# Optimization experiments

Measured on AMD Instinct MI355X. Metric: run time of the kernel, lower is better.

## Reference

```python
import jax, jax.numpy as jnp
import numpy as np

DIM = 384
HEADS = 12
WS = (2, 7, 7)
SS = (1, 3, 3)


def _rel_position_index(ws):
    coords = np.stack(np.meshgrid(np.arange(ws[0]), np.arange(ws[1]), np.arange(ws[2]), indexing='ij'))
    cf = coords.reshape(3, -1)                      # (3, N)
    rc = cf[:, :, None] - cf[:, None, :]            # (3, N, N)
    rc = rc.transpose(1, 2, 0).astype(np.int64)     # (N, N, 3)
    rc[..., 0] += ws[0] - 1
    rc[..., 1] += ws[1] - 1
    rc[..., 2] += ws[2] - 1
    rc[..., 0] *= (2 * ws[1] - 1) * (2 * ws[2] - 1)
    rc[..., 1] *= 2 * ws[2] - 1
    return rc.sum(-1)                               # (N, N)


def _compute_mask(D, H, W, ws, ss):
    img = np.zeros((1, D, H, W, 1), np.float32)
    cnt = 0
    for d in (slice(0, -ws[0]), slice(-ws[0], -ss[0]), slice(-ss[0], None)):
        for h in (slice(0, -ws[1]), slice(-ws[1], -ss[1]), slice(-ss[1], None)):
            for w in (slice(0, -ws[2]), slice(-ws[2], -ss[2]), slice(-ss[2], None)):
                img[:, d, h, w, :] = cnt
                cnt += 1
    x = img.reshape(1, D // ws[0], ws[0], H // ws[1], ws[1], W // ws[2], ws[2], 1)
    mw = x.transpose(0, 1, 3, 5, 2, 4, 6, 7).reshape(-1, ws[0] * ws[1] * ws[2])  # (nW, N)
    am = mw[:, None, :] - mw[:, :, None]
    return jnp.asarray(np.where(am != 0, -100.0, 0.0).astype(np.float32))  # (nW, N, N)


def _window_partition(x, ws):
    B, D, H, W, C = x.shape
    x = x.reshape(B, D // ws[0], ws[0], H // ws[1], ws[1], W // ws[2], ws[2], C)
    return x.transpose(0, 1, 3, 5, 2, 4, 6, 7).reshape(-1, ws[0] * ws[1] * ws[2], C)


def _window_reverse(win, ws, B, D, H, W):
    x = win.reshape(B, D // ws[0], H // ws[1], W // ws[2], ws[0], ws[1], ws[2], -1)
    return x.transpose(0, 1, 4, 2, 5, 3, 6, 7).reshape(B, D, H, W, -1)


def _ln(x, g, b, eps=1e-5):
    mu = x.mean(-1, keepdims=True)
    var = ((x - mu) ** 2).mean(-1, keepdims=True)
    return (x - mu) * jax.lax.rsqrt(var + eps) * g + b


def setup_inputs() -> dict:
    key = jax.random.key(0)
    ks = jax.random.split(key, 8)
    C = DIM
    Ch = int(4.0 * C)
    s = lambda k, shape: jax.random.normal(k, shape, dtype=jnp.float32) * 0.02
    nbias = (2 * WS[0] - 1) * (2 * WS[1] - 1) * (2 * WS[2] - 1)
    return dict(
        x=jax.random.normal(ks[0], (4, 8, 56, 56, C), dtype=jnp.float32),
        norm1_g=jnp.ones((C,), jnp.float32), norm1_b=jnp.zeros((C,), jnp.float32),
        qkv_w=s(ks[1], (3 * C, C)), qkv_b=jnp.zeros((3 * C,), jnp.float32),
        rpb_table=s(ks[2], (nbias, HEADS)),
        proj_w=s(ks[3], (C, C)), proj_b=jnp.zeros((C,), jnp.float32),
        norm2_g=jnp.ones((C,), jnp.float32), norm2_b=jnp.zeros((C,), jnp.float32),
        fc1_w=s(ks[4], (Ch, C)), fc1_b=jnp.zeros((Ch,), jnp.float32),
        fc2_w=s(ks[5], (C, Ch)), fc2_b=jnp.zeros((C,), jnp.float32),
    )


def reference(x, norm1_g, norm1_b, qkv_w, qkv_b, rpb_table, proj_w, proj_b,
              norm2_g, norm2_b, fc1_w, fc1_b, fc2_w, fc2_b):
    B, D, H, W, C = x.shape
    ws, ss = WS, SS
    hd = C // HEADS
    N = ws[0] * ws[1] * ws[2]

    shortcut = x
    h = _ln(x, norm1_g, norm1_b)
    # cyclic shift (no padding needed: D,H,W are window multiples)
    h = jnp.roll(h, shift=(-ss[0], -ss[1], -ss[2]), axis=(1, 2, 3))
    xw = _window_partition(h, ws)                       # (B_, N, C)
    B_ = xw.shape[0]

    qkv = (xw @ qkv_w.T + qkv_b).reshape(B_, N, 3, HEADS, hd).transpose(2, 0, 3, 1, 4)
    q, k, v = qkv[0], qkv[1], qkv[2]                    # (B_, heads, N, hd)
    attn = jnp.einsum('bhnd,bhmd->bhnm', q * (hd ** -0.5), k)

    rpi = _rel_position_index(ws)                       # (N, N) static
    bias = rpb_table[rpi.reshape(-1)].reshape(N, N, HEADS).transpose(2, 0, 1)
    attn = attn + bias[None]

    mask = _compute_mask(D, H, W, ws, ss)               # (nW, N, N)
    nW = mask.shape[0]
    attn = attn.reshape(B_ // nW, nW, HEADS, N, N) + mask[None, :, None]
    attn = jax.nn.softmax(attn.reshape(-1, HEADS, N, N), axis=-1)

    out = jnp.einsum('bhnm,bhmd->bhnd', attn, v).transpose(0, 2, 1, 3).reshape(B_, N, C)
    out = out @ proj_w.T + proj_b

    h = _window_reverse(out, ws, B, D, H, W)
    h = jnp.roll(h, shift=(ss[0], ss[1], ss[2]), axis=(1, 2, 3))
    x = shortcut + h

    y = _ln(x, norm2_g, norm2_b)
    y = jax.nn.gelu(y @ fc1_w.T + fc1_b, approximate=False) @ fc2_w.T + fc2_b
    return x + y
```

## Files before the change

kernel.cpp:

```cpp
#include <hip/hip_runtime.h>
#include <hip/hip_bf16.h>
#include <cmath>

typedef __hip_bfloat16 bf16;
typedef __attribute__((ext_vector_type(8))) short s16x8;
typedef __attribute__((ext_vector_type(4))) float f32x4v;

__device__ __forceinline__ float bf2f(bf16 v){ return __bfloat162float(v); }
__device__ __forceinline__ bf16  f2bf(float v){ return __float2bfloat16(v); }

__device__ __forceinline__ void gload16(const void* g, void* l){
  __builtin_amdgcn_global_load_lds((const __attribute__((address_space(1))) void*)g,
                                   (__attribute__((address_space(3))) void*)l,
                                   16, 0, 0);
}

__device__ __forceinline__ int xcd_swizzle(int bid, int nb){
  int q = nb >> 3, r = nb & 7;
  int xcd = bid & 7, idx = bid >> 3;
  return (xcd < r) ? (xcd*(q+1) + idx) : (r + xcd*q + idx);
}

__device__ __forceinline__ float gelu_f(float v){
  float y = 0.797884561f*(v + 0.044715f*v*v*v);
  float e = __expf(-2.f*y);
  return v * __builtin_amdgcn_rcpf(1.f + e);
}

__global__ void k_f2bf4(const float* __restrict__ s0, const float* __restrict__ s1,
                        const float* __restrict__ s2, const float* __restrict__ s3,
                        bf16* __restrict__ out){
  int i = blockIdx.x*256 + threadIdx.x;
  if (i >= 1769472) return;
  float v;
  if      (i <  442368) v = s0[i];
  else if (i <  589824) v = s1[i -  442368];
  else if (i < 1179648) v = s2[i -  589824];
  else                  v = s3[i - 1179648];
  out[i] = f2bf(v);
}

__global__ void k_comb(const float* __restrict__ rpb, float* __restrict__ comb){
  int idx = blockIdx.x*256 + threadIdx.x;
  int col = idx & 127, row = (idx>>7)&127, clshead = idx>>14;
  int cls = clshead/12, head = clshead - cls*12;
  float v;
  if (row >= 98) v = 0.f;
  else if (col >= 98) v = -10000.f;
  else {
    int qd = row/49, qr = row%49, qh = qr/7, qw = qr%7;
    int kd = col/49, kr = col%49, kh = kr/7, kw = kr%7;
    int pbq = qd*169 + qh*13 + qw;
    int pbk = kd*169 + kh*13 + kw;
    int lq, lk;
    {
      int ld = (cls&4) ? (qd==0?1:2) : 0;
      int lh = (cls&2) ? (qh<4?1:2) : 0;
      int lw = (cls&1) ? (qw<4?1:2) : 0;
      lq = ld*9+lh*3+lw;
    }
    {
      int ld = (cls&4) ? (kd==0?1:2) : 0;
      int lh = (cls&2) ? (kh<4?1:2) : 0;
      int lw = (cls&1) ? (kw<4?1:2) : 0;
      lk = ld*9+lh*3+lw;
    }
    float bias = rpb[(pbq-pbk+253)*12 + head];
    v = bias + ((lq!=lk) ? -100.f : 0.f);
  }
  comb[idx] = v;
}

__global__ __launch_bounds__(256)
void k_ln1(const float* __restrict__ x, const float* __restrict__ g,
           const float* __restrict__ b, bf16* __restrict__ xw, long tbase)
{
  int tl = blockIdx.x*4 + (threadIdx.x>>6);
  long t = tbase + tl;
  int lane = threadIdx.x & 63;
  int win = (int)(t / 98), n = (int)(t % 98);
  int batch = win>>8;
  int wq = win & 7, hq = (win>>3)&7, dq = (win>>6)&3;
  int dr = n/49, rem = n%49, hr = rem/7, wr = rem%7;
  int d = dq*2+dr, h = hq*7+hr, w = wq*7+wr;
  int sd = (d+1)&7;
  int sh = h+3; if (sh>=56) sh-=56;
  int sw = w+3; if (sw>=56) sw-=56;
  const float* row = x + ((size_t)(((batch*8+sd)*56+sh)*56+sw))*384;
  float v[6]; float s=0.f, ss=0.f;
  int c0 = lane*6;
  #pragma unroll
  for (int i=0;i<6;++i){ float f = row[c0+i]; v[i]=f; s+=f; ss+=f*f; }
  #pragma unroll
  for (int o=32;o>0;o>>=1){ s += __shfl_xor(s,o); ss += __shfl_xor(ss,o); }
  float mu = s*(1.f/384.f);
  float var = ss*(1.f/384.f) - mu*mu;
  float rstd = rsqrtf(var + 1e-5f);
  bf16* orow = xw + (size_t)tl*384;
  #pragma unroll
  for (int i=0;i<6;++i){ int c=c0+i; orow[c] = f2bf((v[i]-mu)*rstd*g[c] + b[c]); }
}

template<int EPI, int KT>
__global__ __launch_bounds__(256, 2)
void k_gemm(const bf16* __restrict__ A, const bf16* __restrict__ B,
            const float* __restrict__ bias, const float* __restrict__ resid,
            void* __restrict__ outp, int N, int nx)
{
  constexpr int K = KT*32;
  __shared__ __align__(16) bf16 As[2][256*32];
  __shared__ __align__(16) bf16 Bs[2][128*32];
  const int tid = threadIdx.x;
  const int wave = tid>>6, lane = tid&63;
  const int wg = xcd_swizzle(blockIdx.x, gridDim.x);
  const int tn = wg % nx, tm = wg / nx;
  const int wm = wave>>1, wn = wave&1;
  const int fr = lane & 15, l4 = lane>>4;

  f32x4v acc[8][4];
  #pragma unroll
  for (int i=0;i<8;++i)
    #pragma unroll
    for (int j=0;j<4;++j)
      #pragma unroll
      for (int e=0;e<4;++e) acc[i][j][e] = 0.f;

  const int srow0 = lane>>2;
  const int scol_sw = (((lane&3) ^ ((lane>>3)&3)))*8;
  const bf16* gA = A + ((size_t)tm*256 + wave*16 + srow0)*K + scol_sw;
  const bf16* gB = B + ((size_t)tn*128 + wave*16 + srow0)*K + scol_sw;

  auto stage = [&](int buf, int koff){
    #pragma unroll
    for (int j=0;j<4;++j)
      gload16(gA + (size_t)(64*j)*K + koff, &As[buf][j*2048 + wave*512]);
    #pragma unroll
    for (int j=0;j<2;++j)
      gload16(gB + (size_t)(64*j)*K + koff, &Bs[buf][j*2048 + wave*512]);
  };

  stage(0, 0);

  const int fko_sw = ((l4 ^ ((fr>>1)&3)))*8;

  #pragma unroll 2
  for (int kt=0; kt<KT; ++kt){
    asm volatile("s_waitcnt vmcnt(0) lgkmcnt(0)" ::: "memory");
    __builtin_amdgcn_s_barrier();
    if (kt+1 < KT) stage((kt+1)&1, (kt+1)*32);
    const bf16* Ab = As[kt&1];
    const bf16* Bb = Bs[kt&1];
    s16x8 af[8], bfr[4];
    #pragma unroll
    for (int i=0;i<4;++i)
      bfr[i] = *(const s16x8*)&Bb[(wn*64 + i*16 + fr)*32 + fko_sw];
    #pragma unroll
    for (int i=0;i<8;++i)
      af[i] = *(const s16x8*)&Ab[(wm*128 + i*16 + fr)*32 + fko_sw];
    #pragma unroll
    for (int mi=0;mi<8;++mi)
      #pragma unroll
      for (int ni=0;ni<4;++ni)
        acc[mi][ni] = __builtin_amdgcn_mfma_f32_16x16x32_bf16(af[mi], bfr[ni], acc[mi][ni], 0,0,0);
    __builtin_amdgcn_s_barrier();
  }

  #pragma unroll
  for (int mi=0;mi<8;++mi){
    #pragma unroll
    for (int ni=0;ni<4;++ni){
      int col = tn*128 + wn*64 + ni*16 + fr;
      float bv = bias[col];
      int rowb = tm*256 + wm*128 + mi*16 + l4*4;
      #pragma unroll
      for (int r=0;r<4;++r){
        size_t idx = (size_t)(rowb+r)*N + col;
        float v = acc[mi][ni][r] + bv;
        if (EPI==0){
          ((bf16*)outp)[idx] = f2bf(v);
        } else if (EPI==1){
          ((bf16*)outp)[idx] = f2bf(gelu_f(v));
        } else if (EPI==3){
          if (col < 384) v *= 0.17677669529663687f;
          ((bf16*)outp)[idx] = f2bf(v);
        } else {
          ((float*)outp)[idx] = v + resid[idx];
        }
      }
    }
  }
}

template<int KT>
__global__ __launch_bounds__(512, 1)
void k_projln2(const bf16* __restrict__ A, const bf16* __restrict__ B,
               const float* __restrict__ bias, const float* __restrict__ x,
               const float* __restrict__ g, const float* __restrict__ b2,
               float* __restrict__ outx, bf16* __restrict__ ln2,
               long tbase, long lnbase)
{
  constexpr int K = KT*32;
  __shared__ __align__(16) bf16 As[2][128*32];
  __shared__ __align__(16) bf16 Bs[2][384*32];
  __shared__ float redS[128][4];
  __shared__ float redQ[128][4];
  const int tid = threadIdx.x;
  const int wave = tid>>6, lane = tid&63;
  const int tm = xcd_swizzle(blockIdx.x, gridDim.x);
  const int wm = wave>>2, wn = wave&3;
  const int fr = lane & 15, l4 = lane>>4;

  f32x4v acc[4][6];
  #pragma unroll
  for (int i=0;i<4;++i)
    #pragma unroll
    for (int j=0;j<6;++j)
      #pragma unroll
      for (int e=0;e<4;++e) acc[i][j][e] = 0.f;

  const int srow0 = lane>>2;
  const int scol_sw = (((lane&3) ^ ((lane>>3)&3)))*8;
  const bf16* gA = A + ((size_t)tm*128 + wave*16 + srow0)*K + scol_sw;
  const bf16* gB = B + ((size_t)(wave*16) + srow0)*K + scol_sw;

  auto stage = [&](int buf, int koff){
    gload16(gA + koff, &As[buf][wave*512]);
    #pragma unroll
    for (int j=0;j<3;++j)
      gload16(gB + (size_t)(128*j)*K + koff, &Bs[buf][(j*128 + wave*16)*32]);
  };

  stage(0, 0);
  const int fko_sw = ((l4 ^ ((fr>>1)&3)))*8;

  #pragma unroll 2
  for (int kt=0; kt<KT; ++kt){
    asm volatile("s_waitcnt vmcnt(0) lgkmcnt(0)" ::: "memory");
    __builtin_amdgcn_s_barrier();
    if (kt+1 < KT) stage((kt+1)&1, (kt+1)*32);
    const bf16* Ab = As[kt&1];
    const bf16* Bb = Bs[kt&1];
    s16x8 af[4], bfr[6];
    #pragma unroll
    for (int i=0;i<6;++i)
      bfr[i] = *(const s16x8*)&Bb[(wn*96 + i*16 + fr)*32 + fko_sw];
    #pragma unroll
    for (int i=0;i<4;++i)
      af[i] = *(const s16x8*)&Ab[(wm*64 + i*16 + fr)*32 + fko_sw];
    #pragma unroll
    for (int mi=0;mi<4;++mi)
      #pragma unroll
      for (int ni=0;ni<6;++ni)
        acc[mi][ni] = __builtin_amdgcn_mfma_f32_16x16x32_bf16(af[mi], bfr[ni], acc[mi][ni], 0,0,0);
    __builtin_amdgcn_s_barrier();
  }

  float bv[6];
  #pragma unroll
  for (int ni=0;ni<6;++ni) bv[ni] = bias[wn*96 + ni*16 + fr];

  long nr[4][4];
  #pragma unroll
  for (int mi=0;mi<4;++mi){
    #pragma unroll
    for (int r=0;r<4;++r){
      int lrow = wm*64 + mi*16 + l4*4 + r;
      int ti = (int)(tbase + (long)tm*128 + lrow);
      int win = ti/98, n = ti - win*98;
      int batch = win>>8;
      int wq = win&7, hq = (win>>3)&7, dq = (win>>6)&3;
      int dr = n/49, rem = n - dr*49, hr = rem/7, wr = rem - hr*7;
      int d = dq*2+dr, h = hq*7+hr, w = wq*7+wr;
      int sd = (d+1)&7;
      int sh = h+3; if (sh>=56) sh-=56;
      int sw = w+3; if (sw>=56) sw-=56;
      long nrow = (long)batch*25088 + (long)(sd*56+sh)*56 + sw;
      nr[mi][r] = nrow;
      const float* xrow = x + (size_t)nrow*384;
      float* orow = outx + (size_t)nrow*384;
      float s = 0.f, q = 0.f;
      #pragma unroll
      for (int ni=0;ni<6;++ni){
        int col = wn*96 + ni*16 + fr;
        float hvl = acc[mi][ni][r] + bv[ni] + xrow[col];
        orow[col] = hvl;
        acc[mi][ni][r] = hvl;
        s += hvl; q += hvl*hvl;
      }
      s += __shfl_xor(s,1); q += __shfl_xor(q,1);
      s += __shfl_xor(s,2); q += __shfl_xor(q,2);
      s += __shfl_xor(s,4); q += __shfl_xor(q,4);
      s += __shfl_xor(s,8); q += __shfl_xor(q,8);
      if (fr == 0){ redS[lrow][wn] = s; redQ[lrow][wn] = q; }
    }
  }
  __syncthreads();
  float gv[6], b2v[6];
  #pragma unroll
  for (int ni=0;ni<6;++ni){
    int col = wn*96 + ni*16 + fr;
    gv[ni] = g[col]; b2v[ni] = b2[col];
  }
  #pragma unroll
  for (int mi=0;mi<4;++mi){
    #pragma unroll
    for (int r=0;r<4;++r){
      int lrow = wm*64 + mi*16 + l4*4 + r;
      float S = redS[lrow][0] + redS[lrow][1] + redS[lrow][2] + redS[lrow][3];
      float Q = redQ[lrow][0] + redQ[lrow][1] + redQ[lrow][2] + redQ[lrow][3];
      float mu = S*(1.f/384.f);
      float var = Q*(1.f/384.f) - mu*mu;
      float rstd = rsqrtf(var + 1e-5f);
      bf16* lrowp = ln2 + (size_t)(nr[mi][r] - lnbase)*384;
      #pragma unroll
      for (int ni=0;ni<6;++ni){
        int col = wn*96 + ni*16 + fr;
        lrowp[col] = f2bf((acc[mi][ni][r] - mu)*rstd*gv[ni] + b2v[ni]);
      }
    }
  }
}

__global__ __launch_bounds__(256)
void k_attn(const bf16* __restrict__ qkv, const float* __restrict__ comb,
            bf16* __restrict__ outp)
{
  const int wg   = xcd_swizzle(blockIdx.x, gridDim.x);
  const int head = wg % 12;
  const int win  = wg / 12;
  const int tid  = threadIdx.x;
  const int wave = tid>>6;
  const int lane = tid&63;
  const int l15 = lane & 15, l4 = lane>>4;
  __shared__ __align__(16) bf16 Vt[32*136];
  __shared__ __align__(16) bf16 P_buf[4][16*40];

  const int wq = win&7, hq=(win>>3)&7, dq=(win>>6)&3;
  const int cls = ((dq==3)?4:0) | ((hq==7)?2:0) | ((wq==7)?1:0);
  const float* combbase = comb + (size_t)(cls*12+head)*128*128;
  const bf16* qkvw_ = qkv + (size_t)win*98*1152;

  for (int i = tid; i < 512; i += 256){
    int m = i>>2, d0 = (i&3)*8;
    int mc = m>97 ? 97 : m;
    s16x8 v = *(const s16x8*)(qkvw_ + (size_t)mc*1152 + 384 + 384 + head*32 + d0);
    #pragma unroll
    for (int e=0;e<8;++e){ short sv = v[e]; Vt[(d0+e)*136 + m] = *(bf16*)&sv; }
  }
  s16x8 kb[8];
  #pragma unroll
  for (int j=0;j<8;++j){
    int tok = j*16 + l15; if (tok>97) tok = 97;
    kb[j] = *(const s16x8*)(qkvw_ + (size_t)tok*1152 + 384 + head*32 + l4*8);
  }
  __syncthreads();

  const int c0 = wave*32;
  bf16* Pw = P_buf[wave];
  #pragma unroll
  for (int mi=0;mi<2;++mi){
    int q = c0 + mi*16 + l15; if (q>97) q=97;
    s16x8 aq = *(const s16x8*)(qkvw_ + (size_t)q*1152 + head*32 + l4*8);
    f32x4v s[8];
    const float* cb = combbase + (size_t)(c0+mi*16+l4*4)*128 + l15;
    #pragma unroll
    for (int j=0;j<8;++j){
      f32x4v ci = { cb[j*16], cb[j*16+128], cb[j*16+256], cb[j*16+384] };
      s[j] = __builtin_amdgcn_mfma_f32_16x16x32_bf16(aq, kb[j], ci, 0,0,0);
    }
    float rinv[4];
    #pragma unroll
    for (int r=0;r<4;++r){
      float mx = s[0][r];
      #pragma unroll
      for (int j=1;j<8;++j) mx = fmaxf(mx, s[j][r]);
      mx = fmaxf(mx, __shfl_xor(mx,1));
      mx = fmaxf(mx, __shfl_xor(mx,2));
      mx = fmaxf(mx, __shfl_xor(mx,4));
      mx = fmaxf(mx, __shfl_xor(mx,8));
      float sum = 0.f;
      #pragma unroll
      for (int j=0;j<8;++j){ float e = __expf(s[j][r]-mx); s[j][r]=e; sum+=e; }
      sum += __shfl_xor(sum,1);
      sum += __shfl_xor(sum,2);
      sum += __shfl_xor(sum,4);
      sum += __shfl_xor(sum,8);
      rinv[r] = 1.f/sum;
    }
    f32x4v oacc[2] = {{0.f,0.f,0.f,0.f},{0.f,0.f,0.f,0.f}};
    #pragma unroll
    for (int ks=0; ks<4; ++ks){
      #pragma unroll
      for (int jj=0;jj<2;++jj)
        #pragma unroll
        for (int r=0;r<4;++r)
          Pw[(l4*4+r)*40 + jj*16 + l15] = f2bf(s[ks*2+jj][r]);
      s16x8 pa = *(const s16x8*)&Pw[l15*40 + l4*8];
      #pragma unroll
      for (int ni=0;ni<2;++ni){
        s16x8 vb = *(const s16x8*)&Vt[(ni*16+l15)*136 + ks*32 + l4*8];
        oacc[ni] = __builtin_amdgcn_mfma_f32_16x16x32_bf16(pa, vb, oacc[ni], 0,0,0);
      }
    }
    #pragma unroll
    for (int r=0;r<4;++r){
      int qo = c0 + mi*16 + l4*4 + r;
      if (qo < 98){
        bf16* orow = outp + ((size_t)win*98 + qo)*384 + head*32;
        #pragma unroll
        for (int ni=0;ni<2;++ni)
          orow[ni*16+l15] = f2bf(oacc[ni][r]*rinv[r]);
      }
    }
  }
}

extern "C" void kernel_launch(void* const* d_in, const int* in_sizes, int n_in,
                              void* d_out, int out_size, void* d_ws, size_t ws_size,
                              hipStream_t stream)
{
  const float* x     = (const float*)d_in[0];
  const float* n1g   = (const float*)d_in[1];
  const float* n1b   = (const float*)d_in[2];
  const float* qkvw  = (const float*)d_in[3];
  const float* qkvbv = (const float*)d_in[4];
  const float* rpb   = (const float*)d_in[5];
  const float* projw = (const float*)d_in[6];
  const float* projb = (const float*)d_in[7];
  const float* n2g   = (const float*)d_in[8];
  const float* n2b   = (const float*)d_in[9];
  const float* fc1w  = (const float*)d_in[10];
  const float* fc1b  = (const float*)d_in[11];
  const float* fc2w  = (const float*)d_in[12];
  const float* fc2b  = (const float*)d_in[13];
  float* out = (float*)d_out;

  char* ws = (char*)d_ws;
  size_t off = 0;
  auto alloc = [&](size_t bytes)->char*{
    char* p = ws + off; off += (bytes + 255) & ~(size_t)255; return p;
  };
  bf16*  wall  = (bf16*)alloc((size_t)1769472*2);
  bf16*  wqkv  = wall;
  bf16*  wproj = wall + 442368;
  bf16*  wfc1  = wall + 589824;
  bf16*  wfc2  = wall + 1179648;
  float* comb  = (float*)alloc((size_t)96*128*128*4);

  k_f2bf4<<<(1769472+255)/256,256,0,stream>>>(qkvw, projw, fc1w, fc2w, wall);
  k_comb<<<6144,256,0,stream>>>(rpb, comb);

  const size_t fused_need = off
      + (((size_t)100352*384*2  + 255) & ~(size_t)255)
      + (((size_t)100352*1536*2 + 255) & ~(size_t)255)
      + (((size_t)100352*384*2  + 255) & ~(size_t)255);
  if (ws_size >= fused_need){
    bf16* xw   = (bf16*)alloc((size_t)100352*384*2);
    bf16* bufA = (bf16*)alloc((size_t)100352*1536*2);
    bf16* ln2  = (bf16*)alloc((size_t)100352*384*2);
    bf16* attno = bufA + (size_t)100352*1152;

    k_ln1<<<25088,256,0,stream>>>(x, n1g, n1b, xw, 0L);
    k_gemm<3,12><<<392*9,256,0,stream>>>(xw, wqkv, qkvbv, nullptr, bufA, 1152, 9);
    k_attn<<<12*1024,256,0,stream>>>(bufA, comb, attno);
    k_projln2<12><<<784,512,0,stream>>>(attno, wproj, projb, x, n2g, n2b, out, ln2, 0L, 0L);
    k_gemm<1,12><<<392*12,256,0,stream>>>(ln2, wfc1, fc1b, nullptr, bufA, 1536, 12);
    k_gemm<2,48><<<392*3,256,0,stream>>>(bufA, wfc2, fc2b, out, (void*)out, 384, 3);
  } else {
    bf16* xw   = (bf16*)alloc((size_t)25088*384*2);
    bf16* bufA = (bf16*)alloc((size_t)25088*1536*2);
    bf16* ln2  = (bf16*)alloc((size_t)25088*384*2);
    bf16* attno = bufA + (size_t)25088*1152;
    for (int b=0; b<4; ++b){
      long tbase = (long)b*25088;
      k_ln1<<<6272,256,0,stream>>>(x, n1g, n1b, xw, tbase);
      k_gemm<3,12><<<98*9,256,0,stream>>>(xw, wqkv, qkvbv, nullptr, bufA, 1152, 9);
      k_attn<<<12*256,256,0,stream>>>(bufA, comb, attno);
      k_projln2<12><<<196,512,0,stream>>>(attno, wproj, projb, x, n2g, n2b, out, ln2, tbase, tbase);
      k_gemm<1,12><<<98*12,256,0,stream>>>(ln2, wfc1, fc1b, nullptr, bufA, 1536, 12);
      float* resid = out + (size_t)b*25088*384;
      k_gemm<2,48><<<98*3,256,0,stream>>>(bufA, wfc2, fc2b, resid, (void*)resid, 384, 3);
    }
  }
}
```

Before: 968.3 us.

## Add 256x256 8-wave GEMM kernel for QKV and FC1 with padded QKV weights

Adds a new 512-thread GEMM kernel with 256x256 output tiles and a 64-wide K step. It interleaves LDS fragment loads, next-tile prefetch and MFMA phases separated by barriers and s_setprio. The QKV weight and bias are zero-padded from 1152 to 1280 columns to fit the 256-wide N tile, and the attention kernel now takes the row stride as a parameter. The aim is more data reuse per tile and better overlap of loads with matrix math, at the cost of padding waste, an extra workspace buffer for the attention output, and lower occupancy.

```diff
diff --git a/kernel.cpp b/kernel.cpp
--- a/kernel.cpp
+++ b/kernel.cpp
@@ -38,6 +38,16 @@
   else if (i < 1179648) v = s2[i -  589824];
   else                  v = s3[i - 1179648];
   out[i] = f2bf(v);
+}
+__global__ void k_f2bf_pad(const float* __restrict__ in, bf16* __restrict__ out,
+                           int n_src, int n_tot){
+  int i = blockIdx.x*256 + threadIdx.x;
+  if (i < n_tot) out[i] = (i < n_src) ? f2bf(in[i]) : f2bf(0.f);
+}
+__global__ void k_padb(const float* __restrict__ in, float* __restrict__ out,
+                       int n_src, int n_tot){
+  int i = blockIdx.x*256 + threadIdx.x;
+  if (i < n_tot) out[i] = (i < n_src) ? in[i] : 0.f;
 }
 
 __global__ void k_comb(const float* __restrict__ rpb, float* __restrict__ comb){
@@ -102,6 +112,156 @@
 }
 
 template<int EPI, int KT>
+__global__ __launch_bounds__(512, 1)
+void k_gemm8p(const bf16* __restrict__ A, const bf16* __restrict__ B,
+              const float* __restrict__ bias, void* __restrict__ outp,
+              int N, int nx)
+{
+  constexpr int K = KT*64;
+  __shared__ __align__(16) bf16 As[2][256*64];
+  __shared__ __align__(16) bf16 Bs[2][256*64];
+  const int tid = threadIdx.x;
+  const int wave = tid>>6, lane = tid&63;
+  const int wg = xcd_swizzle(blockIdx.x, gridDim.x);
+  const int tn = wg % nx, tm = wg / nx;
+  const int wm = wave>>2, wn = wave&3;
+  const int fr = lane & 15, l4 = lane>>4;
+
+  f32x4v acc[8][4];
+  #pragma unroll
+  for (int i=0;i<8;++i)
+    #pragma unroll
+    for (int j=0;j<4;++j)
+      #pragma unroll
+      for (int e=0;e<4;++e) acc[i][j][e] = 0.f;
+
+  const int lr8 = lane>>3, lc8 = lane&7;
+  const size_t lane_src = (size_t)lr8*K + (size_t)((lc8 ^ lr8)*8);
+  const bf16* gA = A + ((size_t)tm*256 + wave*8)*K + lane_src;
+  const bf16* gB = B + ((size_t)tn*256 + wave*8)*K + lane_src;
+
+  auto stageA = [&](int buf, int kt, int half){
+    #pragma unroll
+    for (int j=0;j<2;++j)
+      gload16(gA + ((size_t)(half*128 + j*64))*K + kt*64,
+              &As[buf][(half*128 + j*64 + wave*8)*64]);
+  };
+  auto stageB = [&](int buf, int kt, int half){
+    #pragma unroll
+    for (int j=0;j<2;++j)
+      gload16(gB + ((size_t)(half*128 + j*64))*K + kt*64,
+              &Bs[buf][(half*128 + j*64 + wave*8)*64]);
+  };
+
+  const int slot0 = (l4 ^ (fr & 7)) * 8;
+
+  stageA(0,0,0); stageA(0,0,1); stageB(0,0,0); stageB(0,0,1);
+  asm volatile("s_waitcnt vmcnt(0)" ::: "memory");
+  __builtin_amdgcn_s_barrier();
+
+  s16x8 afA[4][2], bf0[2][2], bf1[2][2];
+
+  #pragma unroll 2
+  for (int kt=0; kt<KT; ++kt){
+    const bf16* Ab = As[kt&1];
+    const bf16* Bb = Bs[kt&1];
+    const int st = (kt&1)^1;
+    const bool pf = (kt+1 < KT);
+    #pragma unroll
+    for (int i=0;i<4;++i){
+      int r = wm*128 + i*16 + fr;
+      afA[i][0] = *(const s16x8*)&Ab[r*64 + slot0];
+      afA[i][1] = *(const s16x8*)&Ab[r*64 + (slot0^32)];
+    }
+    #pragma unroll
+    for (int i=0;i<2;++i){
+      int r = wn*64 + i*16 + fr;
+      bf0[i][0] = *(const s16x8*)&Bb[r*64 + slot0];
+      bf0[i][1] = *(const s16x8*)&Bb[r*64 + (slot0^32)];
+    }
+    if (pf){ stageA(st, kt+1, 0); stageA(st, kt+1, 1); }
+    __builtin_amdgcn_s_barrier();
+    __builtin_amdgcn_s_setprio(1);
+    #pragma unroll
+    for (int mi=0;mi<4;++mi)
+      #pragma unroll
+      for (int ni=0;ni<2;++ni)
+        #pragma unroll
+        for (int kk=0;kk<2;++kk)
+          acc[mi][ni] = __builtin_amdgcn_mfma_f32_16x16x32_bf16(afA[mi][kk], bf0[ni][kk], acc[mi][ni], 0,0,0);
+    __builtin_amdgcn_s_setprio(0);
+    __builtin_amdgcn_s_barrier();
+    #pragma unroll
+    for (int i=0;i<2;++i){
+      int r = wn*64 + (i+2)*16 + fr;
+      bf1[i][0] = *(const s16x8*)&Bb[r*64 + slot0];
+      bf1[i][1] = *(const s16x8*)&Bb[r*64 + (slot0^32)];
+    }
+    if (pf){ stageB(st, kt+1, 0); stageB(st, kt+1, 1); }
+    __builtin_amdgcn_s_barrier();
+    __builtin_amdgcn_s_setprio(1);
+    #pragma unroll
+    for (int mi=0;mi<4;++mi)
+      #pragma unroll
+      for (int ni=0;ni<2;++ni)
+        #pragma unroll
+        for (int kk=0;kk<2;++kk)
+          acc[mi][ni+2] = __builtin_amdgcn_mfma_f32_16x16x32_bf16(afA[mi][kk], bf1[ni][kk], acc[mi][ni+2], 0,0,0);
+    __builtin_amdgcn_s_setprio(0);
+    __builtin_amdgcn_s_barrier();
+    #pragma unroll
+    for (int i=0;i<4;++i){
+      int r = wm*128 + (i+4)*16 + fr;
+      afA[i][0] = *(const s16x8*)&Ab[r*64 + slot0];
+      afA[i][1] = *(const s16x8*)&Ab[r*64 + (slot0^32)];
+    }
+    __builtin_amdgcn_s_barrier();
+    __builtin_amdgcn_s_setprio(1);
+    #pragma unroll
+    for (int mi=0;mi<4;++mi)
+      #pragma unroll
+      for (int ni=0;ni<2;++ni)
+        #pragma unroll
+        for (int kk=0;kk<2;++kk)
+          acc[mi+4][ni+2] = __builtin_amdgcn_mfma_f32_16x16x32_bf16(afA[mi][kk], bf1[ni][kk], acc[mi+4][ni+2], 0,0,0);
+    __builtin_amdgcn_s_setprio(0);
+    __builtin_amdgcn_s_barrier();
+    __builtin_amdgcn_s_setprio(1);
+    #pragma unroll
+    for (int mi=0;mi<4;++mi)
+      #pragma unroll
+      for (int ni=0;ni<2;++ni)
+        #pragma unroll
+        for (int kk=0;kk<2;++kk)
+          acc[mi+4][ni] = __builtin_amdgcn_mfma_f32_16x16x32_bf16(afA[mi][kk], bf0[ni][kk], acc[mi+4][ni], 0,0,0);
+    __builtin_amdgcn_s_setprio(0);
+    asm volatile("s_waitcnt vmcnt(0) lgkmcnt(0)" ::: "memory");
+    __builtin_amdgcn_s_barrier();
+  }
+
+  #pragma unroll
+  for (int mi=0;mi<8;++mi){
+    #pragma unroll
+    for (int ni=0;ni<4;++ni){
+      int col = tn*256 + wn*64 + ni*16 + fr;
+      float bv = bias[col];
+      int rowb = tm*256 + wm*128 + mi*16 + l4*4;
+      #pragma unroll
+      for (int r=0;r<4;++r){
+        size_t idx = (size_t)(rowb+r)*N + col;
+        float v = acc[mi][ni][r] + bv;
+        if (EPI==1){
+          ((bf16*)outp)[idx] = f2bf(gelu_f(v));
+        } else {
+          if (col < 384) v *= 0.17677669529663687f;
+          ((bf16*)outp)[idx] = f2bf(v);
+        }
+      }
+    }
+  }
+}
+
+template<int EPI, int KT>
 __global__ __launch_bounds__(256, 2)
 void k_gemm(const bf16* __restrict__ A, const bf16* __restrict__ B,
             const float* __restrict__ bias, const float* __restrict__ resid,
@@ -140,7 +300,6 @@
   };
 
   stage(0, 0);
-
   const int fko_sw = ((l4 ^ ((fr>>1)&3)))*8;
 
   #pragma unroll 2
@@ -323,7 +482,7 @@
 
 __global__ __launch_bounds__(256)
 void k_attn(const bf16* __restrict__ qkv, const float* __restrict__ comb,
-            bf16* __restrict__ outp)
+            bf16* __restrict__ outp, int qs)
 {
   const int wg   = xcd_swizzle(blockIdx.x, gridDim.x);
   const int head = wg % 12;
@@ -338,12 +497,12 @@
   const int wq = win&7, hq=(win>>3)&7, dq=(win>>6)&3;
   const int cls = ((dq==3)?4:0) | ((hq==7)?2:0) | ((wq==7)?1:0);
   const float* combbase = comb + (size_t)(cls*12+head)*128*128;
-  const bf16* qkvw_ = qkv + (size_t)win*98*1152;
+  const bf16* qkvw_ = qkv + (size_t)win*98*qs;
 
   for (int i = tid; i < 512; i += 256){
     int m = i>>2, d0 = (i&3)*8;
     int mc = m>97 ? 97 : m;
-    s16x8 v = *(const s16x8*)(qkvw_ + (size_t)mc*1152 + 384 + 384 + head*32 + d0);
+    s16x8 v = *(const s16x8*)(qkvw_ + (size_t)mc*qs + 768 + head*32 + d0);
     #pragma unroll
     for (int e=0;e<8;++e){ short sv = v[e]; Vt[(d0+e)*136 + m] = *(bf16*)&sv; }
   }
@@ -351,7 +510,7 @@
   #pragma unroll
   for (int j=0;j<8;++j){
     int tok = j*16 + l15; if (tok>97) tok = 97;
-    kb[j] = *(const s16x8*)(qkvw_ + (size_t)tok*1152 + 384 + head*32 + l4*8);
+    kb[j] = *(const s16x8*)(qkvw_ + (size_t)tok*qs + 384 + head*32 + l4*8);
   }
   __syncthreads();
 
@@ -360,7 +519,7 @@
   #pragma unroll
   for (int mi=0;mi<2;++mi){
     int q = c0 + mi*16 + l15; if (q>97) q=97;
-    s16x8 aq = *(const s16x8*)(qkvw_ + (size_t)q*1152 + head*32 + l4*8);
+    s16x8 aq = *(const s16x8*)(qkvw_ + (size_t)q*qs + head*32 + l4*8);
     f32x4v s[8];
     const float* cb = combbase + (size_t)(c0+mi*16+l4*4)*128 + l15;
     #pragma unroll
@@ -441,43 +600,47 @@
     char* p = ws + off; off += (bytes + 255) & ~(size_t)255; return p;
   };
   bf16*  wall  = (bf16*)alloc((size_t)1769472*2);
-  bf16*  wqkv  = wall;
   bf16*  wproj = wall + 442368;
   bf16*  wfc1  = wall + 589824;
   bf16*  wfc2  = wall + 1179648;
+  bf16*  wqkvp = (bf16*)alloc((size_t)1280*384*2);
+  float* qkvbp = (float*)alloc((size_t)1280*4);
   float* comb  = (float*)alloc((size_t)96*128*128*4);
 
   k_f2bf4<<<(1769472+255)/256,256,0,stream>>>(qkvw, projw, fc1w, fc2w, wall);
+  k_f2bf_pad<<<(1280*384+255)/256,256,0,stream>>>(qkvw, wqkvp, 1152*384, 1280*384);
+  k_padb<<<5,256,0,stream>>>(qkvbv, qkvbp, 1152, 1280);
   k_comb<<<6144,256,0,stream>>>(rpb, comb);
 
   const size_t fused_need = off
       + (((size_t)100352*384*2  + 255) & ~(size_t)255)
       + (((size_t)100352*1536*2 + 255) & ~(size_t)255)
+      + (((size_t)100352*384*2  + 255) & ~(size_t)255)
       + (((size_t)100352*384*2  + 255) & ~(size_t)255);
   if (ws_size >= fused_need){
-    bf16* xw   = (bf16*)alloc((size_t)100352*384*2);
-    bf16* bufA = (bf16*)alloc((size_t)100352*1536*2);
-    bf16* ln2  = (bf16*)alloc((size_t)100352*384*2);
-    bf16* attno = bufA + (size_t)100352*1152;
+    bf16* xw    = (bf16*)alloc((size_t)100352*384*2);
+    bf16* bufA  = (bf16*)alloc((size_t)100352*1536*2);
+    bf16* ln2   = (bf16*)alloc((size_t)100352*384*2);
+    bf16* attno = (bf16*)alloc((size_t)100352*384*2);
 
     k_ln1<<<25088,256,0,stream>>>(x, n1g, n1b, xw, 0L);
-    k_gemm<3,12><<<392*9,256,0,stream>>>(xw, wqkv, qkvbv, nullptr, bufA, 1152, 9);
-    k_attn<<<12*1024,256,0,stream>>>(bufA, comb, attno);
+    k_gemm8p<3,6><<<392*5,512,0,stream>>>(xw, wqkvp, qkvbp, bufA, 1280, 5);
+    k_attn<<<12*1024,256,0,stream>>>(bufA, comb, attno, 1280);
     k_projln2<12><<<784,512,0,stream>>>(attno, wproj, projb, x, n2g, n2b, out, ln2, 0L, 0L);
-    k_gemm<1,12><<<392*12,256,0,stream>>>(ln2, wfc1, fc1b, nullptr, bufA, 1536, 12);
+    k_gemm8p<1,6><<<392*6,512,0,stream>>>(ln2, wfc1, fc1b, bufA, 1536, 6);
     k_gemm<2,48><<<392*3,256,0,stream>>>(bufA, wfc2, fc2b, out, (void*)out, 384, 3);
   } else {
-    bf16* xw   = (bf16*)alloc((size_t)25088*384*2);
-    bf16* bufA = (bf16*)alloc((size_t)25088*1536*2);
-    bf16* ln2  = (bf16*)alloc((size_t)25088*384*2);
-    bf16* attno = bufA + (size_t)25088*1152;
+    bf16* xw    = (bf16*)alloc((size_t)25088*384*2);
+    bf16* bufA  = (bf16*)alloc((size_t)25088*1536*2);
+    bf16* ln2   = (bf16*)alloc((size_t)25088*384*2);
+    bf16* attno = (bf16*)alloc((size_t)25088*384*2);
     for (int b=0; b<4; ++b){
       long tbase = (long)b*25088;
       k_ln1<<<6272,256,0,stream>>>(x, n1g, n1b, xw, tbase);
-      k_gemm<3,12><<<98*9,256,0,stream>>>(xw, wqkv, qkvbv, nullptr, bufA, 1152, 9);
-      k_attn<<<12*256,256,0,stream>>>(bufA, comb, attno);
+      k_gemm8p<3,6><<<98*5,512,0,stream>>>(xw, wqkvp, qkvbp, bufA, 1280, 5);
+      k_attn<<<12*256,256,0,stream>>>(bufA, comb, attno, 1280);
       k_projln2<12><<<196,512,0,stream>>>(attno, wproj, projb, x, n2g, n2b, out, ln2, tbase, tbase);
-      k_gemm<1,12><<<98*12,256,0,stream>>>(ln2, wfc1, fc1b, nullptr, bufA, 1536, 12);
+      k_gemm8p<1,6><<<98*6,512,0,stream>>>(ln2, wfc1, fc1b, bufA, 1536, 6);
       float* resid = out + (size_t)b*25088*384;
       k_gemm<2,48><<<98*3,256,0,stream>>>(bufA, wfc2, fc2b, resid, (void*)resid, 384, 3);
     }
```

Result: no change. 982.7 us (+1.5%).

## Retile GEMMs to 128x128 blocks with 64-wide K steps and new LDS swizzle

Applied to the files above, without the earlier changes.

Replaces the 256x128 GEMM tile with a 32-wide K slice by a 128x128 tile that stages a 64-wide K slice per iteration. Each wave now issues two MFMAs per fragment pair per iteration, with an 8-way XOR swizzle on the LDS layout. The trailing barrier in the K loop is dropped, which halves the barriers per element of K. The aim is fewer loop iterations, a smaller accumulator register footprint and twice as many workgroups for better occupancy and load balance, at the cost of less reuse of the B tile per block. The attention kernel also gains a row-stride parameter, which is passed the same value as before.

```diff
diff --git a/kernel.cpp b/kernel.cpp
--- a/kernel.cpp
+++ b/kernel.cpp
@@ -103,13 +103,13 @@
 
 template<int EPI, int KT>
 __global__ __launch_bounds__(256, 2)
-void k_gemm(const bf16* __restrict__ A, const bf16* __restrict__ B,
-            const float* __restrict__ bias, const float* __restrict__ resid,
-            void* __restrict__ outp, int N, int nx)
+void k_gemm64(const bf16* __restrict__ A, const bf16* __restrict__ B,
+              const float* __restrict__ bias, const float* __restrict__ resid,
+              void* __restrict__ outp, int N, int nx)
 {
-  constexpr int K = KT*32;
-  __shared__ __align__(16) bf16 As[2][256*32];
-  __shared__ __align__(16) bf16 Bs[2][128*32];
+  constexpr int K = KT*64;
+  __shared__ __align__(16) bf16 As[2][128*64];
+  __shared__ __align__(16) bf16 Bs[2][128*64];
   const int tid = threadIdx.x;
   const int wave = tid>>6, lane = tid&63;
   const int wg = xcd_swizzle(blockIdx.x, gridDim.x);
@@ -117,61 +117,65 @@
   const int wm = wave>>1, wn = wave&1;
   const int fr = lane & 15, l4 = lane>>4;
 
-  f32x4v acc[8][4];
-  #pragma unroll
-  for (int i=0;i<8;++i)
+  f32x4v acc[4][4];
+  #pragma unroll
+  for (int i=0;i<4;++i)
     #pragma unroll
     for (int j=0;j<4;++j)
       #pragma unroll
       for (int e=0;e<4;++e) acc[i][j][e] = 0.f;
 
-  const int srow0 = lane>>2;
-  const int scol_sw = (((lane&3) ^ ((lane>>3)&3)))*8;
-  const bf16* gA = A + ((size_t)tm*256 + wave*16 + srow0)*K + scol_sw;
-  const bf16* gB = B + ((size_t)tn*128 + wave*16 + srow0)*K + scol_sw;
+  const int lr8 = lane>>3, lc8 = lane&7;
+  const size_t lane_src = (size_t)lr8*K + (size_t)((lc8 ^ lr8)*8);
+  const bf16* gA = A + ((size_t)tm*128 + wave*32)*K + lane_src;
+  const bf16* gB = B + ((size_t)tn*128 + wave*32)*K + lane_src;
 
   auto stage = [&](int buf, int koff){
     #pragma unroll
     for (int j=0;j<4;++j)
-      gload16(gA + (size_t)(64*j)*K + koff, &As[buf][j*2048 + wave*512]);
-    #pragma unroll
-    for (int j=0;j<2;++j)
-      gload16(gB + (size_t)(64*j)*K + koff, &Bs[buf][j*2048 + wave*512]);
+      gload16(gA + (size_t)(j*8)*K + koff, &As[buf][(wave*32 + j*8)*64]);
+    #pragma unroll
+    for (int j=0;j<4;++j)
+      gload16(gB + (size_t)(j*8)*K + koff, &Bs[buf][(wave*32 + j*8)*64]);
   };
 
   stage(0, 0);
 
-  const int fko_sw = ((l4 ^ ((fr>>1)&3)))*8;
+  const int slot0 = (l4 ^ (fr & 7)) * 8;
 
   #pragma unroll 2
   for (int kt=0; kt<KT; ++kt){
     asm volatile("s_waitcnt vmcnt(0) lgkmcnt(0)" ::: "memory");
     __builtin_amdgcn_s_barrier();
-    if (kt+1 < KT) stage((kt+1)&1, (kt+1)*32);
+    if (kt+1 < KT) stage((kt+1)&1, (kt+1)*64);
     const bf16* Ab = As[kt&1];
     const bf16* Bb = Bs[kt&1];
-    s16x8 af[8], bfr[4];
-    #pragma unroll
-    for (int i=0;i<4;++i)
-      bfr[i] = *(const s16x8*)&Bb[(wn*64 + i*16 + fr)*32 + fko_sw];
-    #pragma unroll
-    for (int i=0;i<8;++i)
-      af[i] = *(const s16x8*)&Ab[(wm*128 + i*16 + fr)*32 + fko_sw];
-    #pragma unroll
-    for (int mi=0;mi<8;++mi)
+    s16x8 af[4][2], bfr[4][2];
+    #pragma unroll
+    for (int i=0;i<4;++i){
+      int ra = (wm*64 + i*16 + fr)*64;
+      af[i][0] = *(const s16x8*)&Ab[ra + slot0];
+      af[i][1] = *(const s16x8*)&Ab[ra + (slot0^32)];
+      int rb = (wn*64 + i*16 + fr)*64;
+      bfr[i][0] = *(const s16x8*)&Bb[rb + slot0];
+      bfr[i][1] = *(const s16x8*)&Bb[rb + (slot0^32)];
+    }
+    #pragma unroll
+    for (int mi=0;mi<4;++mi)
       #pragma unroll
       for (int ni=0;ni<4;++ni)
-        acc[mi][ni] = __builtin_amdgcn_mfma_f32_16x16x32_bf16(af[mi], bfr[ni], acc[mi][ni], 0,0,0);
-    __builtin_amdgcn_s_barrier();
-  }
-
-  #pragma unroll
-  for (int mi=0;mi<8;++mi){
+        #pragma unroll
+        for (int kk=0;kk<2;++kk)
+          acc[mi][ni] = __builtin_amdgcn_mfma_f32_16x16x32_bf16(af[mi][kk], bfr[ni][kk], acc[mi][ni], 0,0,0);
+  }
+
+  #pragma unroll
+  for (int mi=0;mi<4;++mi){
     #pragma unroll
     for (int ni=0;ni<4;++ni){
       int col = tn*128 + wn*64 + ni*16 + fr;
       float bv = bias[col];
-      int rowb = tm*256 + wm*128 + mi*16 + l4*4;
+      int rowb = tm*128 + wm*64 + mi*16 + l4*4;
       #pragma unroll
       for (int r=0;r<4;++r){
         size_t idx = (size_t)(rowb+r)*N + col;
@@ -323,7 +327,7 @@
 
 __global__ __launch_bounds__(256)
 void k_attn(const bf16* __restrict__ qkv, const float* __restrict__ comb,
-            bf16* __restrict__ outp)
+            bf16* __restrict__ outp, int qs)
 {
   const int wg   = xcd_swizzle(blockIdx.x, gridDim.x);
   const int head = wg % 12;
@@ -338,12 +342,12 @@
   const int wq = win&7, hq=(win>>3)&7, dq=(win>>6)&3;
   const int cls = ((dq==3)?4:0) | ((hq==7)?2:0) | ((wq==7)?1:0);
   const float* combbase = comb + (size_t)(cls*12+head)*128*128;
-  const bf16* qkvw_ = qkv + (size_t)win*98*1152;
+  const bf16* qkvw_ = qkv + (size_t)win*98*qs;
 
   for (int i = tid; i < 512; i += 256){
     int m = i>>2, d0 = (i&3)*8;
     int mc = m>97 ? 97 : m;
-    s16x8 v = *(const s16x8*)(qkvw_ + (size_t)mc*1152 + 384 + 384 + head*32 + d0);
+    s16x8 v = *(const s16x8*)(qkvw_ + (size_t)mc*qs + 768 + head*32 + d0);
     #pragma unroll
     for (int e=0;e<8;++e){ short sv = v[e]; Vt[(d0+e)*136 + m] = *(bf16*)&sv; }
   }
@@ -351,7 +355,7 @@
   #pragma unroll
   for (int j=0;j<8;++j){
     int tok = j*16 + l15; if (tok>97) tok = 97;
-    kb[j] = *(const s16x8*)(qkvw_ + (size_t)tok*1152 + 384 + head*32 + l4*8);
+    kb[j] = *(const s16x8*)(qkvw_ + (size_t)tok*qs + 384 + head*32 + l4*8);
   }
   __syncthreads();
 
@@ -360,7 +364,7 @@
   #pragma unroll
   for (int mi=0;mi<2;++mi){
     int q = c0 + mi*16 + l15; if (q>97) q=97;
-    s16x8 aq = *(const s16x8*)(qkvw_ + (size_t)q*1152 + head*32 + l4*8);
+    s16x8 aq = *(const s16x8*)(qkvw_ + (size_t)q*qs + head*32 + l4*8);
     f32x4v s[8];
     const float* cb = combbase + (size_t)(c0+mi*16+l4*4)*128 + l15;
     #pragma unroll
@@ -455,31 +459,31 @@
       + (((size_t)100352*1536*2 + 255) & ~(size_t)255)
       + (((size_t)100352*384*2  + 255) & ~(size_t)255);
   if (ws_size >= fused_need){
-    bf16* xw   = (bf16*)alloc((size_t)100352*384*2);
-    bf16* bufA = (bf16*)alloc((size_t)100352*1536*2);
-    bf16* ln2  = (bf16*)alloc((size_t)100352*384*2);
+    bf16* xw    = (bf16*)alloc((size_t)100352*384*2);
+    bf16* bufA  = (bf16*)alloc((size_t)100352*1536*2);
+    bf16* ln2   = (bf16*)alloc((size_t)100352*384*2);
     bf16* attno = bufA + (size_t)100352*1152;
 
     k_ln1<<<25088,256,0,stream>>>(x, n1g, n1b, xw, 0L);
-    k_gemm<3,12><<<392*9,256,0,stream>>>(xw, wqkv, qkvbv, nullptr, bufA, 1152, 9);
-    k_attn<<<12*1024,256,0,stream>>>(bufA, comb, attno);
+    k_gemm64<3,6><<<784*9,256,0,stream>>>(xw, wqkv, qkvbv, nullptr, bufA, 1152, 9);
+    k_attn<<<12*1024,256,0,stream>>>(bufA, comb, attno, 1152);
     k_projln2<12><<<784,512,0,stream>>>(attno, wproj, projb, x, n2g, n2b, out, ln2, 0L, 0L);
-    k_gemm<1,12><<<392*12,256,0,stream>>>(ln2, wfc1, fc1b, nullptr, bufA, 1536, 12);
-    k_gemm<2,48><<<392*3,256,0,stream>>>(bufA, wfc2, fc2b, out, (void*)out, 384, 3);
+    k_gemm64<1,6><<<784*12,256,0,stream>>>(ln2, wfc1, fc1b, nullptr, bufA, 1536, 12);
+    k_gemm64<2,24><<<784*3,256,0,stream>>>(bufA, wfc2, fc2b, out, (void*)out, 384, 3);
   } else {
-    bf16* xw   = (bf16*)alloc((size_t)25088*384*2);
-    bf16* bufA = (bf16*)alloc((size_t)25088*1536*2);
-    bf16* ln2  = (bf16*)alloc((size_t)25088*384*2);
+    bf16* xw    = (bf16*)alloc((size_t)25088*384*2);
+    bf16* bufA  = (bf16*)alloc((size_t)25088*1536*2);
+    bf16* ln2   = (bf16*)alloc((size_t)25088*384*2);
     bf16* attno = bufA + (size_t)25088*1152;
     for (int b=0; b<4; ++b){
       long tbase = (long)b*25088;
       k_ln1<<<6272,256,0,stream>>>(x, n1g, n1b, xw, tbase);
-      k_gemm<3,12><<<98*9,256,0,stream>>>(xw, wqkv, qkvbv, nullptr, bufA, 1152, 9);
-      k_attn<<<12*256,256,0,stream>>>(bufA, comb, attno);
+      k_gemm64<3,6><<<196*9,256,0,stream>>>(xw, wqkv, qkvbv, nullptr, bufA, 1152, 9);
+      k_attn<<<12*256,256,0,stream>>>(bufA, comb, attno, 1152);
       k_projln2<12><<<196,512,0,stream>>>(attno, wproj, projb, x, n2g, n2b, out, ln2, tbase, tbase);
-      k_gemm<1,12><<<98*12,256,0,stream>>>(ln2, wfc1, fc1b, nullptr, bufA, 1536, 12);
+      k_gemm64<1,6><<<196*12,256,0,stream>>>(ln2, wfc1, fc1b, nullptr, bufA, 1536, 12);
       float* resid = out + (size_t)b*25088*384;
-      k_gemm<2,48><<<98*3,256,0,stream>>>(bufA, wfc2, fc2b, resid, (void*)resid, 384, 3);
-    }
-  }
-}
+      k_gemm64<2,24><<<196*3,256,0,stream>>>(bufA, wfc2, fc2b, resid, (void*)resid, 384, 3);
+    }
+  }
+}
```

New measurement: 973.9 us. About the same (+0.6%).
